# Performance work log

Hardware: AMD Instinct MI355X
Metric: run time of the kernel (lower is better)

## Reference

```python
import jax, jax.numpy as jnp
import numpy as np
import math

B, T, H, W, C = 2, 8, 32, 32, 512
DEPTH = 2
HEADS = 16
GH = 8            # global FAVOR+ heads (first GH heads, as in performer-pytorch)
DH = C // HEADS   # 32
WIN = C // 8      # 64 = local window size
FF = 2 * C
NB_F = int(DH * math.log(DH))  # 110 random features (performer default)


def _ortho_proj(m, d, rng):
    # gaussian orthogonal random matrix, scaling=0 (row norms ~ chi(d))
    blocks = []
    for _ in range(m // d + 1):
        q, _ = np.linalg.qr(rng.standard_normal((d, d)))
        blocks.append(q.T)
    Q = np.concatenate(blocks, 0)[:m]
    mult = np.linalg.norm(rng.standard_normal((m, d)), axis=1)
    return (mult[:, None] * Q).astype(np.float32)


def setup_inputs():
    rng = np.random.default_rng(0)
    g = lambda *s: jnp.asarray(rng.standard_normal(s) * 0.02, jnp.float32)
    z = lambda *s: jnp.zeros(s, jnp.float32)
    o = lambda *s: jnp.ones(s, jnp.float32)
    p = {}
    p["x"] = jnp.asarray(rng.standard_normal((B, T, H, W, C)), jnp.float32)
    p["ln1_g"], p["ln1_b"] = o(DEPTH, C), z(DEPTH, C)
    p["Wq"], p["bq"] = g(DEPTH, C, C), z(DEPTH, C)
    p["Wk"], p["bk"] = g(DEPTH, C, C), z(DEPTH, C)
    p["Wv"], p["bv"] = g(DEPTH, C, C), z(DEPTH, C)
    p["Wo"], p["bo"] = g(DEPTH, C, C), z(DEPTH, C)
    p["proj"] = jnp.asarray(np.stack([_ortho_proj(NB_F, DH, rng) for _ in range(DEPTH)]))
    p["ln2_g"], p["ln2_b"] = o(DEPTH, C), z(DEPTH, C)
    p["W1"], p["b1"] = g(DEPTH, C, FF), z(DEPTH, FF)
    p["W2"], p["b2"] = g(DEPTH, FF, C), z(DEPTH, C)
    return p


def _ln(x, g, b):
    m = x.mean(-1, keepdims=True)
    v = x.var(-1, keepdims=True)
    return (x - m) / jnp.sqrt(v + 1e-5) * g + b


def _softmax_kernel(x, proj, is_query):
    # FAVOR+ positive softmax features. x: [b,h,n,d], proj: [m,d]
    d = x.shape[-1]
    m = proj.shape[0]
    dn = d ** -0.25
    dd = jnp.einsum('bhnd,md->bhnm', x * dn, proj)
    diag = jnp.sum(x * x, -1, keepdims=True) * 0.5 * (dn * dn)
    if is_query:
        stab = jnp.max(dd, axis=-1, keepdims=True)
    else:
        stab = jnp.max(dd, axis=(-1, -2), keepdims=True)
    return (m ** -0.5) * (jnp.exp(dd - diag - stab) + 1e-4)


def _rot_half(x):
    x1, x2 = jnp.split(x, 2, axis=-1)
    return jnp.concatenate([-x2, x1], axis=-1)


def _local_attn(q, k, v, win=WIN):
    # non-causal sliding window, look_backward=1, look_forward=1
    b, hh, n, d = q.shape
    nw = n // win
    qb = q.reshape(b, hh, nw, win, d)
    kb = k.reshape(b, hh, nw, win, d)
    vb = v.reshape(b, hh, nw, win, d)

    def look(t):
        p = jnp.pad(t, ((0, 0), (0, 0), (1, 1), (0, 0), (0, 0)))
        return jnp.concatenate([p[:, :, :-2], p[:, :, 1:-1], p[:, :, 2:]], 3)

    kk, vv = look(kb), look(vb)
    posb = jnp.arange(n).reshape(nw, win)
    pp = jnp.pad(posb, ((1, 1), (0, 0)), constant_values=-1)
    kpos = jnp.concatenate([pp[:-2], pp[1:-1], pp[2:]], 1)
    mask = (kpos == -1)[None, None, :, None, :]
    s = jnp.einsum('bhwid,bhwjd->bhwij', qb * (d ** -0.5), kk)
    s = jnp.where(mask, -1e9, s)
    a = jax.nn.softmax(s, axis=-1)
    o = jnp.einsum('bhwij,bhwjd->bhwid', a, vv)
    return o.reshape(b, hh, n, d)


def _forward(x, ln1_g, ln1_b, Wq, bq, Wk, bk, Wv, bv, Wo, bo, proj, ln2_g, ln2_b, W1, b1, W2, b2):
    Bx, Tx, Hx, Wx, Cx = x.shape
    n = Tx * Hx * Wx
    h = x.reshape(Bx, n, Cx)
    # rotary rel-pos for local heads (local-attention rel_pos_emb_config)
    inv_freq = 1.0 / (10000.0 ** (jnp.arange(0, DH, 2, dtype=jnp.float32) / DH))
    freqs = jnp.arange(n, dtype=jnp.float32)[:, None] * inv_freq[None, :]
    emb = jnp.concatenate([freqs, freqs], -1)
    sin, cos = jnp.sin(emb), jnp.cos(emb)

    for l in range(DEPTH):
        y = _ln(h, ln1_g[l], ln1_b[l])
        q = (y @ Wq[l] + bq[l]).reshape(Bx, n, HEADS, DH).transpose(0, 2, 1, 3)
        k = (y @ Wk[l] + bk[l]).reshape(Bx, n, HEADS, DH).transpose(0, 2, 1, 3)
        v = (y @ Wv[l] + bv[l]).reshape(Bx, n, HEADS, DH).transpose(0, 2, 1, 3)
        gq, lq = q[:, :GH], q[:, GH:]
        gk, lk = k[:, :GH], k[:, GH:]
        gv, lv = v[:, :GH], v[:, GH:]
        # global: FAVOR+ linear attention
        qp = _softmax_kernel(gq, proj[l], True)
        kp = _softmax_kernel(gk, proj[l], False)
        Dinv = 1.0 / jnp.einsum('bhnm,bhm->bhn', qp, kp.sum(-2))
        ctx = jnp.einsum('bhnm,bhnd->bhmd', kp, gv)
        og = jnp.einsum('bhmd,bhnm,bhn->bhnd', ctx, qp, Dinv)
        # local: windowed attention with rotary pos emb
        lqr = lq * cos + _rot_half(lq) * sin
        lkr = lk * cos + _rot_half(lk) * sin
        ol = _local_attn(lqr, lkr, lv)
        o = jnp.concatenate([og, ol], 1).transpose(0, 2, 1, 3).reshape(Bx, n, Cx)
        h = h + o @ Wo[l] + bo[l]
        y = _ln(h, ln2_g[l], ln2_b[l])
        h = h + jax.nn.gelu(y @ W1[l] + b1[l], approximate=False) @ W2[l] + b2[l]
    return h.reshape(Bx, Tx, Hx, Wx, Cx)


def reference(x, ln1_g, ln1_b, Wq, bq, Wk, bk, Wv, bv, Wo, bo, proj, ln2_g, ln2_b, W1, b1, W2, b2):
    return _forward(x, ln1_g, ln1_b, Wq, bq, Wk, bk, Wv, bv, Wo, bo, proj, ln2_g, ln2_b, W1, b1, W2, b2)
```

## Files before the change

### kernel.cpp

```cpp
#include <hip/hip_runtime.h>
#include <math.h>

namespace {

constexpr int BATCH = 2;
constexpr int NTOK  = 8192;
constexpr int MROWS = 16384;
constexpr int C     = 512;
constexpr int GH    = 8;
constexpr int DH    = 32;
constexpr int WIN   = 64;
constexpr int NW    = 128;
constexpr int FF    = 1024;
constexpr int NBF   = 110;
constexpr int NBFP  = 128;

constexpr float F_DN     = 0.42044820762685725f;
constexpr float F_RNORM  = 0.09534625892455924f;
constexpr float F_LSCALE = 0.17677669529663687f;

typedef __attribute__((ext_vector_type(8))) short bf16x8;
typedef __attribute__((ext_vector_type(4))) float f32x4;

__device__ __forceinline__ ushort f2b(float f){
  unsigned u = __float_as_uint(f);
  unsigned r = u + 0x7FFFu + ((u >> 16) & 1u);
  return (ushort)(r >> 16);
}
__device__ __forceinline__ float b2f(ushort u){
  return __uint_as_float((unsigned)u << 16);
}

__device__ __forceinline__ void gload16(const void* g, void* l){
  __builtin_amdgcn_global_load_lds((const __attribute__((address_space(1))) void*)g,
                                   (__attribute__((address_space(3))) void*)l, 16, 0, 0);
}

__global__ void k_tables(float* __restrict__ cost, float* __restrict__ sint){
  int idx = blockIdx.x*256 + threadIdx.x;
  if (idx >= NTOK*16) return;
  int pos = idx >> 4, f = idx & 15;
  float inv = powf(10000.f, -(float)f/16.f);
  float ang = (float)pos * inv;
  cost[idx] = cosf(ang);
  sint[idx] = sinf(ang);
}

__global__ __launch_bounds__(256) void k_wcvt_all(const float* __restrict__ Wq, const float* __restrict__ Wk,
     const float* __restrict__ Wv, const float* __restrict__ Wo, const float* __restrict__ W1,
     const float* __restrict__ W2, ushort* __restrict__ wt){
  __shared__ float t[32][33];
  int id = blockIdx.x;
  int l = id >> 11;
  int r = id & 2047;
  const float* src; ushort* dst; int K, N, bx, by;
  if (r < 1024){
    int mat = r >> 8, tt = r & 255;
    bx = tt & 15; by = tt >> 4; K = 512; N = 512;
    src = ((mat == 0) ? Wq : (mat == 1) ? Wk : (mat == 2) ? Wv : Wo) + (size_t)l*262144;
    dst = wt + (size_t)l*2097152 + (size_t)mat*262144;
  } else if (r < 1536){
    int tt = r - 1024;
    bx = tt & 31; by = tt >> 5; K = 512; N = 1024;
    src = W1 + (size_t)l*524288;
    dst = wt + (size_t)l*2097152 + 1048576;
  } else {
    int tt = r - 1536;
    bx = tt & 15; by = tt >> 4; K = 1024; N = 512;
    src = W2 + (size_t)l*524288;
    dst = wt + (size_t)l*2097152 + 1572864;
  }
  int tx = threadIdx.x & 31, ty = threadIdx.x >> 5;
  #pragma unroll
  for (int rr = ty; rr < 32; rr += 8) t[rr][tx] = src[(size_t)(by*32+rr)*N + bx*32 + tx];
  __syncthreads();
  #pragma unroll
  for (int rr = ty; rr < 32; rr += 8) dst[(size_t)(bx*32+rr)*K + by*32 + tx] = f2b(t[tx][rr]);
}

template<int INBF>
__global__ __launch_bounds__(256) void k_ln(const void* __restrict__ xv, const float* __restrict__ g,
                     const float* __restrict__ b, ushort* __restrict__ y){
  int row = blockIdx.x, t = threadIdx.x;
  float2 v;
  if (INBF){
    ushort2 u = *(const ushort2*)((const ushort*)xv + (size_t)row*C + 2*t);
    v.x = b2f(u.x); v.y = b2f(u.y);
  } else {
    v = *(const float2*)((const float*)xv + (size_t)row*C + 2*t);
  }
  float s = v.x + v.y, ss = v.x*v.x + v.y*v.y;
  #pragma unroll
  for (int o = 32; o; o >>= 1){ s += __shfl_down(s, o); ss += __shfl_down(ss, o); }
  __shared__ float rs[4], rss[4];
  int wv = t >> 6, ln = t & 63;
  if (ln == 0){ rs[wv] = s; rss[wv] = ss; }
  __syncthreads();
  float S = rs[0]+rs[1]+rs[2]+rs[3], SS = rss[0]+rss[1]+rss[2]+rss[3];
  float mean = S * (1.f/C);
  float var  = SS * (1.f/C) - mean*mean;
  float rstd = rsqrtf(var + 1e-5f);
  float2 gg = *(const float2*)(g + 2*t);
  float2 bb = *(const float2*)(b + 2*t);
  ushort2 ov;
  ov.x = f2b((v.x - mean)*rstd*gg.x + bb.x);
  ov.y = f2b((v.y - mean)*rstd*gg.y + bb.y);
  *(ushort2*)(y + (size_t)row*C + 2*t) = ov;
}

template<int ACT, int OBF, int QKV, int RESBF>
__global__ __launch_bounds__(512) void k_mgemm(const ushort* __restrict__ A, const ushort* __restrict__ Bt,
      const float* __restrict__ bias, const float* __restrict__ bias2, const float* __restrict__ bias3,
      const void* __restrict__ res, float* __restrict__ outf, ushort* __restrict__ outb,
      const float* __restrict__ cosT, const float* __restrict__ sinT, int Nd, int Kd){
  __shared__ ushort As[2][256*32];
  __shared__ ushort Bs[2][128*32];
  int tid = threadIdx.x;
  int lane = tid & 63, wave = tid >> 6;
  int c = lane & 15, g = lane >> 4;
  int wr = wave >> 1, wc = wave & 1;
  int gx = gridDim.x;
  int nwg = gx * (int)gridDim.y;
  int bid = (int)(blockIdx.y*gx + blockIdx.x);
  int swz = (bid & 7)*(nwg >> 3) + (bid >> 3);
  int row0 = (swz / gx)*256, col0 = (swz % gx)*128;
  f32x4 acc[4][4] = {};
  int nt = Kd >> 5;

  #define STAGE(buf, kt) {                                                        \
    int k0_ = (kt)*32;                                                            \
    _Pragma("unroll")                                                             \
    for (int j = 0; j < 2; j++){                                                  \
      int ci = j*512 + tid;                                                       \
      gload16(A + (size_t)(row0 + (ci>>2))*Kd + k0_ + (ci&3)*8,                   \
              (char*)As[buf] + (j*512 + wave*64)*16);                             \
    }                                                                             \
    {                                                                             \
      int ci = tid;                                                               \
      gload16(Bt + (size_t)(col0 + (ci>>2))*Kd + k0_ + (ci&3)*8,                  \
              (char*)Bs[buf] + (wave*64)*16);                                     \
    }                                                                             \
  }

  STAGE(0, 0);
  __syncthreads();

  for (int t = 0; t < nt; t++){
    int cur = t & 1;
    bf16x8 af[4], bfr[4];
    #pragma unroll
    for (int m = 0; m < 4; m++)
      af[m] = *(const bf16x8*)(As[cur] + (wr*64 + m*16 + c)*32 + g*8);
    #pragma unroll
    for (int n = 0; n < 4; n++)
      bfr[n] = *(const bf16x8*)(Bs[cur] + (wc*64 + n*16 + c)*32 + g*8);
    if (t + 1 < nt) STAGE(cur^1, t+1);
    __builtin_amdgcn_s_setprio(1);
    #pragma unroll
    for (int m = 0; m < 4; m++)
      #pragma unroll
      for (int n = 0; n < 4; n++)
        acc[m][n] = __builtin_amdgcn_mfma_f32_16x16x32_bf16(af[m], bfr[n], acc[m][n], 0, 0, 0);
    __builtin_amdgcn_s_setprio(0);
    __syncthreads();
  }
  #undef STAGE

  if (QKV){
    #pragma unroll
    for (int m = 0; m < 4; m++){
      int rbase = row0 + wr*64 + m*16 + g*4;
      #pragma unroll
      for (int np = 0; np < 2; np++){
        int n0 = 2*np, n1 = n0 + 1;
        int ccol = col0 + wc*64 + n0*16 + c;
        int bid2 = ccol >> 9;
        int cl  = ccol & 511;
        const float* bp = (bid2 == 0) ? bias : (bid2 == 1) ? bias2 : bias3;
        float b0 = bp[cl], b1 = bp[cl+16];
        bool dorope = (bid2 < 2) && (cl >= 256);
        ushort* obase = outb + (size_t)bid2*MROWS*C;
        #pragma unroll
        for (int r = 0; r < 4; r++){
          int grow = rbase + r;
          float a  = acc[m][n0][r] + b0;
          float bb = acc[m][n1][r] + b1;
          if (dorope){
            int pos = grow & (NTOK-1);
            float cv = cosT[pos*16 + c], sv = sinT[pos*16 + c];
            float na = a*cv - bb*sv;
            float nb = bb*cv + a*sv;
            a = na; bb = nb;
          }
          obase[(size_t)grow*C + cl]      = f2b(a);
          obase[(size_t)grow*C + cl + 16] = f2b(bb);
        }
      }
    }
    return;
  }
  #pragma unroll
  for (int m = 0; m < 4; m++){
    int rbase = row0 + wr*64 + m*16 + g*4;
    #pragma unroll
    for (int n = 0; n < 4; n++){
      int ccol = col0 + wc*64 + n*16 + c;
      float bv = bias[ccol];
      #pragma unroll
      for (int r = 0; r < 4; r++){
        int grow = rbase + r;
        float vv = acc[m][n][r] + bv;
        if (ACT == 1) vv = 0.5f*vv*(1.f + erff(vv*0.7071067811865476f));
        if (res){
          size_t ri = (size_t)grow*Nd + ccol;
          vv += RESBF ? b2f(((const ushort*)res)[ri]) : ((const float*)res)[ri];
        }
        if (OBF) outb[(size_t)grow*Nd + ccol] = f2b(vv);
        else     outf[(size_t)grow*Nd + ccol] = vv;
      }
    }
  }
}

__global__ __launch_bounds__(256) void k_ctx3(const ushort* __restrict__ k, const ushort* __restrict__ v,
        const float* __restrict__ proj, float* __restrict__ ctxp, float* __restrict__ ksump){
  int bh = blockIdx.x >> 5, chunk = blockIdx.x & 31;
  int b = bh >> 3, h = bh & 7;
  __shared__ __align__(16) ushort pl[NBFP*40];
  __shared__ __align__(16) ushort Ps[NBFP*72];
  __shared__ __align__(16) ushort Vt[48*72];
  __shared__ float dgl[256];
  int tid = threadIdx.x;
  int lane = tid & 63, wave = tid >> 6;
  int c = lane & 15, g = lane >> 4;
  int i0 = chunk*256;

  for (int idx = tid; idx < NBFP*32; idx += 256){
    int f = idx >> 5, d = idx & 31;
    pl[f*40 + d] = (f < NBF) ? f2b(proj[f*32 + d]*F_DN) : (ushort)0;
  }
  const ushort* kbase = k + ((size_t)b*NTOK + i0)*C + h*DH;
  const ushort* vbase = v + ((size_t)b*NTOK + i0)*C + h*DH;
  #pragma unroll
  for (int s = 0; s < 4; s++){
    bf16x8 kf = *(const bf16x8*)(kbase + (size_t)(s*64 + wave*16 + c)*C + g*8);
    const ushort* kp_ = (const ushort*)&kf;
    float sq = 0.f;
    #pragma unroll
    for (int j = 0; j < 8; j++){ float vv = b2f(kp_[j]); sq += vv*vv; }
    sq += __shfl_xor(sq, 16);
    sq += __shfl_xor(sq, 32);
    if (g == 0) dgl[s*64 + wave*16 + c] = 0.5f*F_DN*F_DN*sq;
  }
  for (int idx = tid; idx < 15*72; idx += 256) Vt[33*72 + idx] = 0;

  f32x4 zz = {0.f, 0.f, 0.f, 0.f};
  f32x4 acc[2][3] = {};

  for (int s = 0; s < 4; s++){
    __syncthreads();
    {
      int r = tid >> 2, part = tid & 3;
      uint4 vv = *(const uint4*)(vbase + (size_t)(s*64 + r)*C + part*8);
      const ushort* vp = (const ushort*)&vv;
      #pragma unroll
      for (int j = 0; j < 8; j++) Vt[(part*8+j)*72 + r] = vp[j];
      if (tid < 64) Vt[32*72 + tid] = 0x3F80;
    }
    bf16x8 af = *(const bf16x8*)(kbase + (size_t)(s*64 + wave*16 + c)*C + g*8);
    #pragma unroll
    for (int ft = 0; ft < 8; ft++){
      bf16x8 bf = *(const bf16x8*)(pl + (ft*16 + c)*40 + g*8);
      f32x4 dd = __builtin_amdgcn_mfma_f32_16x16x32_bf16(af, bf, zz, 0, 0, 0);
      int feat = ft*16 + c;
      bool fvalid = feat < NBF;
      ushort pb[4];
      #pragma unroll
      for (int r = 0; r < 4; r++){
        float kp = 0.f;
        if (fvalid){
          float dg_ = dgl[s*64 + wave*16 + g*4 + r];
          kp = F_RNORM*(__expf(dd[r] - dg_) + 1e-4f);
        }
        pb[r] = f2b(kp);
      }
      uint2 pd;
      pd.x = (unsigned)pb[0] | ((unsigned)pb[1] << 16);
      pd.y = (unsigned)pb[2] | ((unsigned)pb[3] << 16);
      *(uint2*)(Ps + (ft*16 + c)*72 + wave*16 + g*4) = pd;
    }
    __syncthreads();
    #pragma unroll
    for (int i = 0; i < 2; i++){
      int ft = wave*2 + i;
      #pragma unroll
      for (int kk = 0; kk < 2; kk++){
        bf16x8 ap = *(const bf16x8*)(Ps + (ft*16 + c)*72 + kk*32 + g*8);
        #pragma unroll
        for (int nt = 0; nt < 3; nt++){
          bf16x8 bv = *(const bf16x8*)(Vt + (nt*16 + c)*72 + kk*32 + g*8);
          acc[i][nt] = __builtin_amdgcn_mfma_f32_16x16x32_bf16(ap, bv, acc[i][nt], 0, 0, 0);
        }
      }
    }
  }
  size_t pbase = (size_t)(bh*32 + chunk)*NBF;
  #pragma unroll
  for (int i = 0; i < 2; i++){
    int ftb = (wave*2 + i)*16;
    #pragma unroll
    for (int r = 0; r < 4; r++){
      int feat = ftb + g*4 + r;
      if (feat < NBF){
        #pragma unroll
        for (int nt = 0; nt < 2; nt++)
          ctxp[(pbase + feat)*DH + nt*16 + c] = acc[i][nt][r];
        if (c == 0) ksump[pbase + feat] = acc[i][2][r];
      }
    }
  }
}

__global__ void k_ctxred(const float* __restrict__ ctxp, const float* __restrict__ ksump,
                         float* __restrict__ ctx, float* __restrict__ ksum){
  int bh = blockIdx.x / NBF, m = blockIdx.x % NBF;
  int t = threadIdx.x;
  if (t < DH){
    float s = 0.f;
    for (int c = 0; c < 32; c++) s += ctxp[((size_t)(bh*32 + c)*NBF + m)*DH + t];
    ctx[((size_t)bh*NBF + m)*DH + t] = s;
  } else if (t == DH){
    float s = 0.f;
    for (int c = 0; c < 32; c++) s += ksump[(size_t)(bh*32 + c)*NBF + m];
    ksum[bh*NBF + m] = s;
  }
}

__global__ __launch_bounds__(256) void k_qattn3(const ushort* __restrict__ q, const float* __restrict__ proj,
        const float* __restrict__ ctx, const float* __restrict__ ksum, ushort* __restrict__ o){
  int bh = blockIdx.x >> 7, chunk = blockIdx.x & 127;
  int b = bh >> 3, h = bh & 7;
  __shared__ __align__(16) ushort pl[NBFP*40];
  __shared__ __align__(16) ushort ql[64*40];
  __shared__ __align__(16) ushort ctl[32*136];
  __shared__ __align__(16) ushort Ps[64*136];
  __shared__ float ksl[NBFP];
  __shared__ float dgl[64];
  __shared__ float dvl[64];
  int tid = threadIdx.x;
  int lane = tid & 63, wave = tid >> 6;
  int c = lane & 15, g = lane >> 4;
  int i0 = chunk*64;

  for (int idx = tid; idx < NBFP*32; idx += 256){
    int f = idx >> 5, d = idx & 31;
    pl[f*40 + d] = (f < NBF) ? f2b(proj[f*32 + d]*F_DN) : (ushort)0;
  }
  {
    int row = tid >> 2, part = tid & 3;
    uint4 qq = *(const uint4*)(q + (size_t)(b*NTOK + i0 + row)*C + h*DH + part*8);
    *(uint4*)(ql + row*40 + part*8) = qq;
    const ushort* qp_ = (const ushort*)&qq;
    float sq = 0.f;
    #pragma unroll
    for (int j = 0; j < 8; j++){ float vv = b2f(qp_[j]); sq += vv*vv; }
    sq += __shfl_xor(sq, 1);
    sq += __shfl_xor(sq, 2);
    if (part == 0) dgl[row] = 0.5f*F_DN*F_DN*sq;
  }
  for (int idx = tid; idx < 32*NBFP; idx += 256){
    int d = idx >> 7, f = idx & 127;
    float vv = (f < NBF) ? ctx[((size_t)bh*NBF + f)*DH + d] : 0.f;
    ctl[d*136 + f] = f2b(vv);
  }
  if (tid < NBFP) ksl[tid] = (tid < NBF) ? ksum[bh*NBF + tid] : 0.f;
  __syncthreads();

  f32x4 zz = {0.f, 0.f, 0.f, 0.f};
  bf16x8 qf = *(const bf16x8*)(ql + (wave*16 + c)*40 + g*8);
  f32x4 st[8];
  #pragma unroll
  for (int mt = 0; mt < 8; mt++){
    bf16x8 af = *(const bf16x8*)(pl + (mt*16 + c)*40 + g*8);
    st[mt] = __builtin_amdgcn_mfma_f32_16x16x32_bf16(af, qf, zz, 0, 0, 0);
  }
  float mx = -1e30f;
  #pragma unroll
  for (int mt = 0; mt < 8; mt++)
    #pragma unroll
    for (int r = 0; r < 4; r++){
      int feat = mt*16 + g*4 + r;
      if (feat < NBF) mx = fmaxf(mx, st[mt][r]);
    }
  mx = fmaxf(mx, __shfl_xor(mx, 16));
  mx = fmaxf(mx, __shfl_xor(mx, 32));
  float diagv = dgl[wave*16 + c];
  float dv = 0.f;
  #pragma unroll
  for (int mt = 0; mt < 8; mt++){
    ushort pb[4];
    #pragma unroll
    for (int r = 0; r < 4; r++){
      int feat = mt*16 + g*4 + r;
      float qp = 0.f;
      if (feat < NBF) qp = F_RNORM*(__expf(st[mt][r] - diagv - mx) + 1e-4f);
      ushort qb = f2b(qp);
      pb[r] = qb;
      dv += b2f(qb)*ksl[feat];
    }
    uint2 pd;
    pd.x = (unsigned)pb[0] | ((unsigned)pb[1] << 16);
    pd.y = (unsigned)pb[2] | ((unsigned)pb[3] << 16);
    *(uint2*)(Ps + (wave*16 + c)*136 + mt*16 + g*4) = pd;
  }
  dv += __shfl_xor(dv, 16);
  dv += __shfl_xor(dv, 32);
  if (g == 0) dvl[wave*16 + c] = 1.f/dv;
  __syncthreads();

  #pragma unroll
  for (int n = 0; n < 2; n++){
    f32x4 acc = zz;
    #pragma unroll
    for (int kk = 0; kk < 4; kk++){
      bf16x8 ap = *(const bf16x8*)(Ps  + (wave*16 + c)*136 + kk*32 + g*8);
      bf16x8 bc = *(const bf16x8*)(ctl + (n*16 + c)*136    + kk*32 + g*8);
      acc = __builtin_amdgcn_mfma_f32_16x16x32_bf16(ap, bc, acc, 0, 0, 0);
    }
    #pragma unroll
    for (int r = 0; r < 4; r++){
      int qrow = wave*16 + g*4 + r;
      float val = acc[r]*dvl[qrow];
      o[(size_t)(b*NTOK + i0 + qrow)*C + h*DH + n*16 + c] = f2b(val);
    }
  }
}

__global__ __launch_bounds__(256) void k_local2(const ushort* __restrict__ q, const ushort* __restrict__ k,
        const ushort* __restrict__ v, ushort* __restrict__ o){
  int blk = blockIdx.x;
  int w = blk & (NW-1);
  int rem = blk >> 7;
  int hl = rem & 7, b = rem >> 3;
  int hd = GH + hl;
  __shared__ __align__(16) ushort Ks[192*32];
  __shared__ __align__(16) ushort Vt[32*200];
  __shared__ __align__(16) ushort Ps[4*16*200];
  int tid = threadIdx.x;
  int lane = tid & 63, wave = tid >> 6;
  int c = lane & 15, g = lane >> 4;

  const ushort* kbase = k + (size_t)b*NTOK*C + hd*DH;
  const ushort* vbase = v + (size_t)b*NTOK*C + hd*DH;
  #pragma unroll
  for (int s = 0; s < 3; s++){
    int ch = tid + s*256;
    int row = ch >> 2, part = ch & 3;
    int kp = min(max((w-1)*WIN + row, 0), NTOK-1);
    gload16(kbase + (size_t)kp*C + part*8, (char*)Ks + (s*256 + wave*64)*16);
  }
  #pragma unroll
  for (int s = 0; s < 3; s++){
    int ch = tid + s*256;
    int row = ch >> 2, part = ch & 3;
    int kp = min(max((w-1)*WIN + row, 0), NTOK-1);
    uint4 vv = *(const uint4*)(vbase + (size_t)kp*C + part*8);
    const ushort* vp = (const ushort*)&vv;
    #pragma unroll
    for (int j = 0; j < 8; j++) Vt[(part*8+j)*200 + row] = vp[j];
  }
  int qrow = w*WIN + wave*16 + c;
  bf16x8 qf = *(const bf16x8*)(q + ((size_t)b*NTOK + qrow)*C + hd*DH + g*8);
  asm volatile("s_waitcnt vmcnt(0)" ::: "memory");
  __syncthreads();

  f32x4 zz = {0.f, 0.f, 0.f, 0.f};
  f32x4 st[12];
  #pragma unroll
  for (int t = 0; t < 12; t++){
    bf16x8 af = *(const bf16x8*)(Ks + (16*t + c)*32 + g*8);
    st[t] = __builtin_amdgcn_mfma_f32_16x16x32_bf16(af, qf, zz, 0, 0, 0);
  }
  int t0 = (w == 0) ? 4 : 0;
  int t1 = (w == NW-1) ? 8 : 12;
  float lsum = 0.f;
  ushort* pw = Ps + wave*3200 + c*200;
  #pragma unroll
  for (int t = 0; t < 12; t++){
    bool valid = (t >= t0) && (t < t1);
    float p0 = valid ? __expf(st[t][0]*F_LSCALE) : 0.f;
    float p1 = valid ? __expf(st[t][1]*F_LSCALE) : 0.f;
    float p2 = valid ? __expf(st[t][2]*F_LSCALE) : 0.f;
    float p3 = valid ? __expf(st[t][3]*F_LSCALE) : 0.f;
    lsum += (p0+p1)+(p2+p3);
    uint2 pd;
    pd.x = (unsigned)f2b(p0) | ((unsigned)f2b(p1) << 16);
    pd.y = (unsigned)f2b(p2) | ((unsigned)f2b(p3) << 16);
    *(uint2*)(pw + 16*t + 4*g) = pd;
  }
  lsum += __shfl_xor(lsum, 16);
  lsum += __shfl_xor(lsum, 32);

  f32x4 oc0 = zz, oc1 = zz;
  #pragma unroll
  for (int kb = 0; kb < 6; kb++){
    bf16x8 pf = *(const bf16x8*)(pw + kb*32 + g*8);
    bf16x8 v0 = *(const bf16x8*)(Vt + c*200 + kb*32 + g*8);
    bf16x8 v1 = *(const bf16x8*)(Vt + (16 + c)*200 + kb*32 + g*8);
    oc0 = __builtin_amdgcn_mfma_f32_16x16x32_bf16(v0, pf, oc0, 0, 0, 0);
    oc1 = __builtin_amdgcn_mfma_f32_16x16x32_bf16(v1, pf, oc1, 0, 0, 0);
  }
  float inv = 1.f/lsum;
  ushort* orow = o + ((size_t)b*NTOK + qrow)*C + hd*DH;
  uint2 w0, w1;
  w0.x = (unsigned)f2b(oc0[0]*inv) | ((unsigned)f2b(oc0[1]*inv) << 16);
  w0.y = (unsigned)f2b(oc0[2]*inv) | ((unsigned)f2b(oc0[3]*inv) << 16);
  w1.x = (unsigned)f2b(oc1[0]*inv) | ((unsigned)f2b(oc1[1]*inv) << 16);
  w1.y = (unsigned)f2b(oc1[2]*inv) | ((unsigned)f2b(oc1[3]*inv) << 16);
  *(uint2*)(orow + 4*g)      = w0;
  *(uint2*)(orow + 16 + 4*g) = w1;
}

}

extern "C" void kernel_launch(void* const* d_in, const int* in_sizes, int n_in,
                              void* d_out, int out_size, void* d_ws, size_t ws_size,
                              hipStream_t stream){
  (void)in_sizes; (void)n_in; (void)out_size; (void)ws_size;
  const float* x     = (const float*)d_in[0];
  const float* ln1_g = (const float*)d_in[1];
  const float* ln1_b = (const float*)d_in[2];
  const float* Wq    = (const float*)d_in[3];
  const float* bq    = (const float*)d_in[4];
  const float* Wk    = (const float*)d_in[5];
  const float* bk    = (const float*)d_in[6];
  const float* Wv    = (const float*)d_in[7];
  const float* bv    = (const float*)d_in[8];
  const float* Wo    = (const float*)d_in[9];
  const float* bo    = (const float*)d_in[10];
  const float* proj  = (const float*)d_in[11];
  const float* ln2_g = (const float*)d_in[12];
  const float* ln2_b = (const float*)d_in[13];
  const float* W1    = (const float*)d_in[14];
  const float* b1    = (const float*)d_in[15];
  const float* W2    = (const float*)d_in[16];
  const float* b2    = (const float*)d_in[17];

  float* h = (float*)d_out;
  const size_t MC = (size_t)MROWS*C;
  char* w = (char*)d_ws;
  auto alloc = [&](size_t bytes)->char*{ char* p = w; w += (bytes + 255) & ~(size_t)255; return p; };

  ushort* y16  = (ushort*)alloc(MC*2);
  ushort* qb16 = (ushort*)alloc(MC*2);
  ushort* kb16 = (ushort*)alloc(MC*2);
  ushort* vb16 = (ushort*)alloc(MC*2);
  ushort* o16  = (ushort*)alloc(MC*2);
  ushort* h16  = (ushort*)alloc(MC*2);
  ushort* wt   = (ushort*)alloc((size_t)2*2097152*2);
  float*  cost = (float*) alloc((size_t)NTOK*16*4);
  float*  sint = (float*) alloc((size_t)NTOK*16*4);
  float*  ctxb = (float*) alloc((size_t)16*NBF*DH*4);
  float*  ksum = (float*) alloc((size_t)16*NBF*4);

  ushort* mid16 = qb16;
  float*  ctxp  = (float*)o16;
  float*  ksump = ctxp + (size_t)16*32*NBF*DH;

  k_tables<<<(NTOK*16 + 255)/256, 256, 0, stream>>>(cost, sint);
  k_wcvt_all<<<4096, 256, 0, stream>>>(Wq, Wk, Wv, Wo, W1, W2, wt);

  dim3 blkg(512);
  dim3 g512(4, 64);
  dim3 gqkv(12, 64);
  dim3 gff(8, 64);

  for (int l = 0; l < 2; l++){
    const float* pj = proj + (size_t)l*NBF*DH;
    ushort* wl  = wt + (size_t)l*2097152;
    ushort* wtq = wl;
    ushort* wto = wl +  786432;
    ushort* wt1 = wl + 1048576;
    ushort* wt2 = wl + 1572864;

    if (l == 0) k_ln<0><<<MROWS, 256, 0, stream>>>(x,   ln1_g + l*C, ln1_b + l*C, y16);
    else        k_ln<1><<<MROWS, 256, 0, stream>>>(h16, ln1_g + l*C, ln1_b + l*C, y16);
    k_mgemm<0,1,1,0><<<gqkv, blkg, 0, stream>>>(y16, wtq, bq + l*C, bk + l*C, bv + l*C,
                                                nullptr, nullptr, qb16, cost, sint, 1536, C);
    k_ctx3<<<16*32, 256, 0, stream>>>(kb16, vb16, pj, ctxp, ksump);
    k_ctxred<<<16*NBF, 64, 0, stream>>>(ctxp, ksump, ctxb, ksum);
    k_qattn3<<<16*128, 256, 0, stream>>>(qb16, pj, ctxb, ksum, o16);
    k_local2<<<BATCH*8*NW, 256, 0, stream>>>(qb16, kb16, vb16, o16);
    if (l == 0)
      k_mgemm<0,1,0,0><<<g512, blkg, 0, stream>>>(o16, wto, bo + l*C, nullptr, nullptr,
                                                  x, nullptr, h16, nullptr, nullptr, C, C);
    else
      k_mgemm<0,1,0,1><<<g512, blkg, 0, stream>>>(o16, wto, bo + l*C, nullptr, nullptr,
                                                  h16, nullptr, h16, nullptr, nullptr, C, C);
    k_ln<1><<<MROWS, 256, 0, stream>>>(h16, ln2_g + l*C, ln2_b + l*C, y16);
    k_mgemm<1,1,0,0><<<gff, blkg, 0, stream>>>(y16, wt1, b1 + l*FF, nullptr, nullptr, nullptr,
                                               nullptr, mid16, nullptr, nullptr, FF, C);
    if (l == 0)
      k_mgemm<0,1,0,1><<<g512, blkg, 0, stream>>>(mid16, wt2, b2 + l*C, nullptr, nullptr,
                                                  h16, nullptr, h16, nullptr, nullptr, C, FF);
    else
      k_mgemm<0,0,0,1><<<g512, blkg, 0, stream>>>(mid16, wt2, b2 + l*C, nullptr, nullptr,
                                                  h16, h, nullptr, nullptr, nullptr, C, FF);
  }
}
```

Baseline: 479.8 us.

## Add smaller 128x128-tile GEMM kernel for N=512 projections to raise occupancy

Adds a new 256-thread GEMM kernel with 128x128 tiles, double-buffered LDS staging and an XCD-aware block swizzle. It is used for the output projection and the second FFN matmul, both with N=512, replacing the larger-tile 512-thread kernel. The grid doubles from 256 to 512 workgroups, so the 256 CUs are better filled where the old launch gave roughly one block per CU. The trade-off is less operand reuse per tile and more A-matrix reads.

```diff
diff --git a/kernel.cpp b/kernel.cpp
--- a/kernel.cpp
+++ b/kernel.cpp
@@ -222,6 +222,83 @@
   }
 }
 
+template<int ACT, int OBF, int RESBF>
+__global__ __launch_bounds__(256) void k_mgemm_s(const ushort* __restrict__ A, const ushort* __restrict__ Bt,
+      const float* __restrict__ bias, const void* __restrict__ res,
+      float* __restrict__ outf, ushort* __restrict__ outb, int Nd, int Kd){
+  __shared__ ushort As[2][128*32];
+  __shared__ ushort Bs[2][128*32];
+  int tid = threadIdx.x;
+  int lane = tid & 63, wave = tid >> 6;
+  int wr = wave >> 1, wc = wave & 1;
+  int gx = gridDim.x;
+  int nwg = gx * (int)gridDim.y;
+  int bid = (int)(blockIdx.y*gx + blockIdx.x);
+  int swz = (bid & 7)*(nwg >> 3) + (bid >> 3);
+  int row0 = (swz / gx)*128, col0 = (swz % gx)*128;
+  f32x4 acc[4][4] = {};
+  int nt = Kd >> 5;
+
+  #define STAGE(buf, kt) {                                                        \
+    int k0_ = (kt)*32;                                                            \
+    _Pragma("unroll")                                                             \
+    for (int cc = 0; cc < 2; cc++){                                               \
+      int off = (wave*2 + cc)*1024 + lane*16;                                     \
+      int r_ = off >> 6, ke_ = (off & 63) >> 1;                                   \
+      gload16(A  + (size_t)(row0 + r_)*Kd + k0_ + ke_,                            \
+              (char*)As[buf] + (wave*2 + cc)*1024);                               \
+      gload16(Bt + (size_t)(col0 + r_)*Kd + k0_ + ke_,                            \
+              (char*)Bs[buf] + (wave*2 + cc)*1024);                               \
+    }                                                                             \
+  }
+
+  STAGE(0, 0);
+  __syncthreads();
+
+  for (int t = 0; t < nt; t++){
+    int cur = t & 1;
+    bf16x8 af[4], bfr[4];
+    #pragma unroll
+    for (int m = 0; m < 4; m++)
+      af[m] = *(const bf16x8*)((const char*)As[cur] + (wr*64 + m*16 + (lane&15))*64 + (lane>>4)*16);
+    #pragma unroll
+    for (int n = 0; n < 4; n++)
+      bfr[n] = *(const bf16x8*)((const char*)Bs[cur] + (wc*64 + n*16 + (lane&15))*64 + (lane>>4)*16);
+    if (t + 1 < nt) STAGE(cur^1, t+1);
+    __builtin_amdgcn_s_setprio(1);
+    #pragma unroll
+    for (int m = 0; m < 4; m++)
+      #pragma unroll
+      for (int n = 0; n < 4; n++)
+        acc[m][n] = __builtin_amdgcn_mfma_f32_16x16x32_bf16(af[m], bfr[n], acc[m][n], 0, 0, 0);
+    __builtin_amdgcn_s_setprio(0);
+    __syncthreads();
+  }
+  #undef STAGE
+
+  #pragma unroll
+  for (int m = 0; m < 4; m++){
+    int rbase = row0 + wr*64 + m*16 + (lane>>4)*4;
+    #pragma unroll
+    for (int n = 0; n < 4; n++){
+      int ccol = col0 + wc*64 + n*16 + (lane&15);
+      float bv = bias[ccol];
+      #pragma unroll
+      for (int r = 0; r < 4; r++){
+        int grow = rbase + r;
+        float vv = acc[m][n][r] + bv;
+        if (ACT == 1) vv = 0.5f*vv*(1.f + erff(vv*0.7071067811865476f));
+        if (res){
+          size_t ri = (size_t)grow*Nd + ccol;
+          vv += RESBF ? b2f(((const ushort*)res)[ri]) : ((const float*)res)[ri];
+        }
+        if (OBF) outb[(size_t)grow*Nd + ccol] = f2b(vv);
+        else     outf[(size_t)grow*Nd + ccol] = vv;
+      }
+    }
+  }
+}
+
 __global__ __launch_bounds__(256) void k_ctx3(const ushort* __restrict__ k, const ushort* __restrict__ v,
         const float* __restrict__ proj, float* __restrict__ ctxp, float* __restrict__ ksump){
   int bh = blockIdx.x >> 5, chunk = blockIdx.x & 31;
@@ -571,7 +648,8 @@
   k_wcvt_all<<<4096, 256, 0, stream>>>(Wq, Wk, Wv, Wo, W1, W2, wt);
 
   dim3 blkg(512);
-  dim3 g512(4, 64);
+  dim3 blks(256);
+  dim3 g512s(4, 128);
   dim3 gqkv(12, 64);
   dim3 gff(8, 64);
 
@@ -592,19 +670,15 @@
     k_qattn3<<<16*128, 256, 0, stream>>>(qb16, pj, ctxb, ksum, o16);
     k_local2<<<BATCH*8*NW, 256, 0, stream>>>(qb16, kb16, vb16, o16);
     if (l == 0)
-      k_mgemm<0,1,0,0><<<g512, blkg, 0, stream>>>(o16, wto, bo + l*C, nullptr, nullptr,
-                                                  x, nullptr, h16, nullptr, nullptr, C, C);
+      k_mgemm_s<0,1,0><<<g512s, blks, 0, stream>>>(o16, wto, bo + l*C, x, nullptr, h16, C, C);
     else
-      k_mgemm<0,1,0,1><<<g512, blkg, 0, stream>>>(o16, wto, bo + l*C, nullptr, nullptr,
-                                                  h16, nullptr, h16, nullptr, nullptr, C, C);
+      k_mgemm_s<0,1,1><<<g512s, blks, 0, stream>>>(o16, wto, bo + l*C, h16, nullptr, h16, C, C);
     k_ln<1><<<MROWS, 256, 0, stream>>>(h16, ln2_g + l*C, ln2_b + l*C, y16);
     k_mgemm<1,1,0,0><<<gff, blkg, 0, stream>>>(y16, wt1, b1 + l*FF, nullptr, nullptr, nullptr,
                                                nullptr, mid16, nullptr, nullptr, FF, C);
     if (l == 0)
-      k_mgemm<0,1,0,1><<<g512, blkg, 0, stream>>>(mid16, wt2, b2 + l*C, nullptr, nullptr,
-                                                  h16, nullptr, h16, nullptr, nullptr, C, FF);
+      k_mgemm_s<0,1,1><<<g512s, blks, 0, stream>>>(mid16, wt2, b2 + l*C, h16, nullptr, h16, C, FF);
     else
-      k_mgemm<0,0,0,1><<<g512, blkg, 0, stream>>>(mid16, wt2, b2 + l*C, nullptr, nullptr,
-                                                  h16, h, nullptr, nullptr, nullptr, C, FF);
-  }
-}
+      k_mgemm_s<0,0,1><<<g512s, blks, 0, stream>>>(mid16, wt2, b2 + l*C, h16, h, nullptr, C, FF);
+  }
+}
```

Result: no change. 477.4 us (-0.5%).
